# Performance work log

Hardware: AMD Instinct MI355X
Metric: run time of the kernel (lower is better)

Reference implementation:

```python
import jax, jax.numpy as jnp
import numpy as np
from itertools import combinations

WAY = 5
TSS = 3  # temporal_set_size


def setup_inputs() -> dict:
    key = jax.random.key(0)
    k1, k2, k3 = jax.random.split(key, 3)
    n_support, n_queries, seq_len, D = 25, 400, 8, 2048
    d_out = D // 2
    support_set = jax.random.normal(k1, (n_support, seq_len, D), dtype=jnp.float32)
    queries = jax.random.normal(k2, (n_queries, seq_len, D), dtype=jnp.float32)
    support_labels = jnp.arange(n_support, dtype=jnp.int64) % WAY  # shot=5 per class
    W = jax.random.normal(k3, (d_out, TSS * D), dtype=jnp.float32) * 0.02
    b = jnp.zeros((d_out,), dtype=jnp.float32)
    return {"support_set": support_set, "support_labels": support_labels,
            "queries": queries, "W": W, "b": b}


def reference(support_set, support_labels, queries, W, b):
    # Dropout is identity at inference; omitted for determinism.
    n_s, seq_len, D = support_set.shape
    n_q = queries.shape[0]
    tup = jnp.asarray(list(combinations(range(seq_len), TSS)))  # [Tn, 3]
    Tn = tup.shape[0]
    # gather frame tuples and flatten: [N, Tn, 3*D]
    s = support_set[:, tup, :].reshape(n_s, Tn, TSS * D)
    q = queries[:, tup, :].reshape(n_q, Tn, TSS * D)
    # Linear + ReLU embedding
    qe = jax.nn.relu(q.reshape(n_q * Tn, TSS * D) @ W.T + b)          # [Q*Tn, d2]
    se = jax.nn.relu(s.reshape(n_s * Tn, TSS * D) @ W.T + b)
    se = se.reshape(n_s, Tn, -1)
    # group support by class (labels are static ints; shot per class is equal)
    order = jnp.argsort(support_labels, stable=True)                  # sorted by label
    cls_se = se[order.reshape(WAY, -1)].reshape(WAY, -1, se.shape[-1])  # [way, shot*Tn, d2]
    # pairwise Euclidean distances per class: ||q||^2 + ||s||^2 - 2 q.s
    q2 = jnp.sum(qe * qe, axis=-1)                                    # [Q*Tn]
    s2 = jnp.sum(cls_se * cls_se, axis=-1)                            # [way, shot*Tn]
    dots = jnp.einsum('qd,csd->cqs', qe, cls_se)                      # [way, Q*Tn, shot*Tn]
    dist = jnp.sqrt(jnp.maximum(q2[None, :, None] + s2[:, None, :] - 2.0 * dots, 0.0))
    min_dist = dist.min(axis=2).reshape(WAY, n_q, Tn)                 # min over class supports
    logits = -min_dist.mean(axis=2).T                                 # [n_q, way]
    return logits
```

## Files before the change

### kernel.cpp

```cpp
#include <hip/hip_runtime.h>
#include <math.h>

#define NSUP 25
#define NQ   400
#define SL   8
#define DIM  2048
#define DOUT 1024
#define WAY  5
#define TN   56
#define SHOT 5
#define QT   (NQ*TN)
#define STC  (SHOT*TN)
#define NFS  (NSUP*SL)
#define NFQ  (NQ*SL)
#define MF   (NFS+NFQ)
#define MFP  3456
#define PN   (3*DOUT)
#define NSE  1400
#define NSEP 1408

typedef __attribute__((ext_vector_type(8))) short short8;
typedef __attribute__((ext_vector_type(8))) int   int8v;
typedef __attribute__((ext_vector_type(4))) float f32x4;

#define GLOAD_LDS(g, l) __builtin_amdgcn_global_load_lds( \
    (const __attribute__((address_space(1))) unsigned*)(g), \
    (__attribute__((address_space(3))) unsigned*)(l), 16, 0, 0)

__device__ __forceinline__ unsigned short f2bf(float x) {
  unsigned u = __float_as_uint(x);
  u += 0x7fff + ((u >> 16) & 1);
  return (unsigned short)(u >> 16);
}
__device__ __forceinline__ float bf2f(unsigned short h) {
  return __uint_as_float(((unsigned)h) << 16);
}
__device__ __forceinline__ unsigned pk4_fp8(float a, float b, float c, float d) {
  unsigned p = __builtin_amdgcn_cvt_pk_fp8_f32(a, b, 0, false);
  p = __builtin_amdgcn_cvt_pk_fp8_f32(c, d, p, true);
  return p;
}
__device__ __forceinline__ float f8deq(unsigned b) {
  unsigned e = (b >> 3) & 15, m = b & 7;
  return e ? ldexpf((float)(8 + m), (int)e - 10) : ldexpf((float)m, -9);
}

__device__ __constant__ unsigned short TUP[TN] = {
  0x210,0x310,0x410,0x510,0x610,0x710,
  0x320,0x420,0x520,0x620,0x720,
  0x430,0x530,0x630,0x730,
  0x540,0x640,0x740,
  0x650,0x750,
  0x760,
  0x321,0x421,0x521,0x621,0x721,
  0x431,0x531,0x631,0x731,
  0x541,0x641,0x741,
  0x651,0x751,
  0x761,
  0x432,0x532,0x632,0x732,
  0x542,0x642,0x742,
  0x652,0x752,
  0x762,
  0x543,0x643,0x743,
  0x653,0x753,
  0x763,
  0x654,0x754,
  0x764,
  0x765
};

__global__ __launch_bounds__(256) void prep(
    const float* __restrict__ sup, const float* __restrict__ qry,
    const float* __restrict__ W,
    unsigned char* __restrict__ A8, unsigned char* __restrict__ W8,
    unsigned char* __restrict__ se8, float* __restrict__ s2,
    unsigned* __restrict__ pmin)
{
  int idx = blockIdx.x * 256 + threadIdx.x;
  {
    int e = idx * 4;
    int row = e >> 11, c = e & 2047;
    float4 v = make_float4(0.f, 0.f, 0.f, 0.f);
    if (row < NFS)      v = *(const float4*)(sup + (size_t)row * DIM + c);
    else if (row < MF)  v = *(const float4*)(qry + (size_t)(row - NFS) * DIM + c);
    *(unsigned*)(A8 + e) = pk4_fp8(v.x, v.y, v.z, v.w);
  }
  if (idx < PN*DIM/4) {
    int e = idx * 4;
    int n = e >> 11, c = e & 2047;
    const float4 v = *(const float4*)(W + (size_t)(n & 1023) * (3*DIM) + (n >> 10) * DIM + c);
    *(unsigned*)(W8 + e) = pk4_fp8(v.x*64.f, v.y*64.f, v.z*64.f, v.w*64.f);
  }
  if (idx < WAY * QT) pmin[idx] = 0x7F800000u;
  if (idx < (NSEP - NSE) * DOUT) se8[(size_t)NSE * DOUT + idx] = 0;
  if (idx < NSEP - NSE) s2[NSE + idx] = 0.f;
}

__device__ __forceinline__ void mfma_kloop_f8(
    const unsigned char* pa, const unsigned char* pb, int sa, int sb,
    unsigned char* As, unsigned char* Bs,
    int w, int l, int nk, int wm, int wn, int lane15, int quad, f32x4 acc[4][4])
{
  const int r0 = w*32 + (l >> 3), cb = (l & 7) * 16;
  pa += (size_t)r0 * sa + cb;
  pb += (size_t)r0 * sb + cb;
  unsigned char* lA = As + (w*32) * 128;
  unsigned char* lB = Bs + (w*32) * 128;
  for (int kk = 0; kk < nk; ++kk) {
    __syncthreads();
#pragma unroll
    for (int q = 0; q < 4; ++q) {
      GLOAD_LDS(pa + (size_t)q*8*sa, lA + q*1024);
      GLOAD_LDS(pb + (size_t)q*8*sb, lB + q*1024);
    }
    pa += 128; pb += 128;
    __syncthreads();
    int8v af[4], bfr[4];
#pragma unroll
    for (int i = 0; i < 4; ++i) {
      af[i]  = *(const int8v*)(As + (wm + i*16 + lane15)*128 + quad*32);
      bfr[i] = *(const int8v*)(Bs + (wn + i*16 + lane15)*128 + quad*32);
    }
#pragma unroll
    for (int i = 0; i < 4; ++i)
#pragma unroll
      for (int j = 0; j < 4; ++j)
        acc[i][j] = __builtin_amdgcn_mfma_scale_f32_16x16x128_f8f6f4(
            af[i], bfr[j], acc[i][j], 0, 0, 0, 0x7f7f7f7f, 0, 0x7f7f7f7f);
  }
}

__global__ __launch_bounds__(256) void gemm_embed_f8(
    const unsigned char* __restrict__ A8, const unsigned char* __restrict__ W8,
    unsigned short* __restrict__ P)
{
  __shared__ unsigned char As[128*128];
  __shared__ unsigned char Bs[128*128];
  const int bm = blockIdx.x * 128, bn = blockIdx.y * 128;
  const int tid = threadIdx.x, w = tid >> 6, l = tid & 63;
  const int lane15 = l & 15, quad = l >> 4;
  const int wm = (w & 1) * 64, wn = (w >> 1) * 64;

  f32x4 acc[4][4] = {};
  mfma_kloop_f8(A8 + (size_t)bm * DIM, W8 + (size_t)bn * DIM, DIM, DIM,
                As, Bs, w, l, DIM/128, wm, wn, lane15, quad, acc);

#pragma unroll
  for (int i = 0; i < 4; ++i) {
#pragma unroll
    for (int r = 0; r < 4; ++r) {
      int row = bm + wm + i*16 + quad*4 + r;
      if (row < MF) {
#pragma unroll
        for (int j = 0; j < 4; ++j) {
          int col = bn + wn + j*16 + lane15;
          P[(size_t)row * PN + col] = f2bf(acc[i][j][r] * 0.015625f);
        }
      }
    }
  }
}

__global__ __launch_bounds__(256) void assemble_seq(
    const unsigned short* __restrict__ P, const float* __restrict__ bias,
    unsigned char* __restrict__ qe8, float* __restrict__ q2,
    unsigned char* __restrict__ se8, float* __restrict__ s2)
{
  __shared__ unsigned short sP[SL * PN];
  const int b2 = blockIdx.x, b = b2 >> 1, half = b2 & 1;
  const int tid = threadIdx.x, w = tid >> 6, l = tid & 63;

  const size_t base = (size_t)b * SL * PN;
#pragma unroll
  for (int qi = 0; qi < 12; ++qi) {
    int off = (qi * 256 + tid) * 8;
    *(short8*)&sP[off] = *(const short8*)(P + base + off);
  }
  __syncthreads();

  float4 bbv[4];
#pragma unroll
  for (int c = 0; c < 4; ++c)
    bbv[c] = *(const float4*)&bias[l*4 + c*256];

  const bool is_sup = b < NSUP;
  unsigned char* E = is_sup ? se8 : qe8;
  float* nrm = is_sup ? s2 : q2;
  int row_base;
  if (is_sup) { int cc = b % WAY, kk = b / WAY; row_base = cc * STC + kk * TN; }
  else        { row_base = (b - NSUP) * TN; }

  const int t_end = half * 28 + 28;
  for (int t = half * 28 + w; t < t_end; t += 4) {
    unsigned int tp = TUP[t];
    int f0 = tp & 15, f1 = (tp >> 4) & 15, f2 = (tp >> 8) & 15;
    int row = row_base + t;
    float ssq = 0.f;
#pragma unroll
    for (int c = 0; c < 4; ++c) {
      int o = l*4 + c*256;
      ushort4 a = *(const ushort4*)&sP[f0*PN + o];
      ushort4 bq = *(const ushort4*)&sP[f1*PN + DOUT + o];
      ushort4 d = *(const ushort4*)&sP[f2*PN + 2*DOUT + o];
      float z0 = fmaxf(bf2f(a.x) + bf2f(bq.x) + bf2f(d.x) + bbv[c].x, 0.f);
      float z1 = fmaxf(bf2f(a.y) + bf2f(bq.y) + bf2f(d.y) + bbv[c].y, 0.f);
      float z2 = fmaxf(bf2f(a.z) + bf2f(bq.z) + bf2f(d.z) + bbv[c].z, 0.f);
      float z3 = fmaxf(bf2f(a.w) + bf2f(bq.w) + bf2f(d.w) + bbv[c].w, 0.f);
      unsigned pk = pk4_fp8(z0, z1, z2, z3);
      *(unsigned*)&E[(size_t)row * DOUT + o] = pk;
      float x0 = f8deq(pk & 255),         x1 = f8deq((pk >> 8) & 255);
      float x2 = f8deq((pk >> 16) & 255), x3 = f8deq(pk >> 24);
      ssq += x0*x0 + x1*x1 + x2*x2 + x3*x3;
    }
#pragma unroll
    for (int off = 1; off < 64; off <<= 1) ssq += __shfl_xor(ssq, off, 64);
    if (l == 0) nrm[row] = ssq;
  }
}

__global__ __launch_bounds__(256) void gemm_dist_f8(
    const unsigned char* __restrict__ qe8, const unsigned char* __restrict__ se8,
    const float* __restrict__ q2, const float* __restrict__ s2,
    unsigned* __restrict__ pmin)
{
  __shared__ unsigned char As[128*128];
  __shared__ unsigned char Bs[128*128];
  const int bm = blockIdx.x * 128;
  const int bn = blockIdx.y * 128;
  const int tid = threadIdx.x, w = tid >> 6, l = tid & 63;
  const int lane15 = l & 15, quad = l >> 4;
  const int wm = (w & 1) * 64, wn = (w >> 1) * 64;

  f32x4 acc[4][4] = {};
  mfma_kloop_f8(se8 + (size_t)bm * DOUT, qe8 + (size_t)bn * DOUT, DOUT, DOUT,
                As, Bs, w, l, DOUT/128, wm, wn, lane15, quad, acc);

  float s2v[4][4]; int clsv[4][4];
#pragma unroll
  for (int i = 0; i < 4; ++i)
#pragma unroll
    for (int r = 0; r < 4; ++r) {
      int sec = bm + wm + i*16 + quad*4 + r;
      s2v[i][r] = s2[sec];
      clsv[i][r] = sec / STC;
    }
#pragma unroll
  for (int i = 0; i < 4; ++i)
#pragma unroll
    for (int j = 0; j < 4; ++j)
#pragma unroll
      for (int r = 0; r < 4; ++r)
        acc[i][j][r] = fmaf(-2.f, acc[i][j][r], s2v[i][r]);

  float q2v[4];
#pragma unroll
  for (int j = 0; j < 4; ++j)
    q2v[j] = q2[bn + wn + j*16 + lane15];

  const int c_lo = (bm + wm) / STC;
  const int c_hi = min((bm + wm + 63) / STC, WAY - 1);
  for (int c = c_lo; c <= c_hi; ++c) {
#pragma unroll
    for (int j = 0; j < 4; ++j) {
      float mv = INFINITY;
#pragma unroll
      for (int i = 0; i < 4; ++i)
#pragma unroll
        for (int r = 0; r < 4; ++r)
          mv = fminf(mv, (clsv[i][r] == c) ? acc[i][j][r] : INFINITY);
      mv = fminf(mv, __shfl_xor(mv, 16, 64));
      mv = fminf(mv, __shfl_xor(mv, 32, 64));
      if (quad == 0) {
        float val = fmaxf(q2v[j] + mv, 0.f);
        atomicMin(&pmin[(size_t)c * QT + bn + wn + j*16 + lane15],
                  __float_as_uint(val));
      }
    }
  }
}

__global__ void finalize(const unsigned* __restrict__ pmin, float* __restrict__ out)
{
  int idx = blockIdx.x * blockDim.x + threadIdx.x;
  if (idx >= NQ * WAY) return;
  int i = idx / WAY, c = idx % WAY;
  float sum = 0.f;
  for (int t = 0; t < TN; ++t) {
    float v = __uint_as_float(pmin[(size_t)c * QT + i * TN + t]);
    sum += sqrtf(v);
  }
  out[i * WAY + c] = -sum * (1.f / (float)TN);
}

extern "C" void kernel_launch(void* const* d_in, const int* in_sizes, int n_in,
                              void* d_out, int out_size, void* d_ws, size_t ws_size,
                              hipStream_t stream) {
  const float* support = (const float*)d_in[0];
  const float* queries  = (const float*)d_in[2];
  const float* W        = (const float*)d_in[3];
  const float* bias     = (const float*)d_in[4];
  float* out = (float*)d_out;

  char* ws = (char*)d_ws;
  unsigned char* A8 = (unsigned char*)ws;           ws += (size_t)MFP * DIM;
  unsigned char* W8 = (unsigned char*)ws;           ws += (size_t)PN * DIM;
  unsigned short* P = (unsigned short*)ws;          ws += (size_t)MF * PN * 2;
  unsigned char* qe8 = (unsigned char*)ws;          ws += (size_t)QT * DOUT;
  unsigned char* se8 = (unsigned char*)ws;          ws += (size_t)NSEP * DOUT;
  float*         q2  = (float*)ws;                  ws += (size_t)QT * 4;
  float*         s2  = (float*)ws;                  ws += (size_t)NSEP * 4;
  unsigned*      pm  = (unsigned*)ws;

  prep<<<MFP*DIM/4/256, 256, 0, stream>>>(support, queries, W, A8, W8, se8, s2, pm);
  gemm_embed_f8<<<dim3(MFP/128, PN/128), 256, 0, stream>>>(A8, W8, P);
  assemble_seq<<<2*(NSUP + NQ), 256, 0, stream>>>(P, bias, qe8, q2, se8, s2);
  gemm_dist_f8<<<dim3(NSEP/128, QT/128), 256, 0, stream>>>(qe8, se8, q2, s2, pm);
  finalize<<<(NQ*WAY + 255)/256, 256, 0, stream>>>(pm, out);
}
```

Baseline: 220.5 us.

## Use 256x128 FP8 GEMM tiles with swizzled LDS layout and B-fragment reuse

Both FP8 MFMA GEMMs (embedding and distance) now use 256-row A tiles with 8x4 accumulators per wave, which halves the number of blocks and raises arithmetic intensity per LDS load. The LDS layout gets an XOR column swizzle to reduce bank conflicts on fragment reads. B fragments are now loaded one at a time and reused across eight MFMAs. Padding grows and rows are clamped so the larger tiles stay in bounds. The cost is more registers per thread (launch_bounds 256,2), more LDS per block, and fewer blocks, which may under-fill the GPU for the distance GEMM's 6-wide grid.

```diff
diff --git a/kernel.cpp b/kernel.cpp
--- a/kernel.cpp
+++ b/kernel.cpp
@@ -14,7 +14,7 @@
 #define NFS  (NSUP*SL)
 #define NFQ  (NQ*SL)
 #define MF   (NFS+NFQ)
-#define MFP  3456
+#define MFP  3584
 #define PN   (3*DOUT)
 #define NSE  1400
 #define NSEP 1408
@@ -97,56 +97,65 @@
 }
 
 __device__ __forceinline__ void mfma_kloop_f8(
-    const unsigned char* pa, const unsigned char* pb, int sa, int sb,
+    const unsigned char* __restrict__ gA, const unsigned char* __restrict__ gB,
+    int sa, int sb, int rowA0, int rowB0, int clampA,
     unsigned char* As, unsigned char* Bs,
-    int w, int l, int nk, int wm, int wn, int lane15, int quad, f32x4 acc[4][4])
-{
-  const int r0 = w*32 + (l >> 3), cb = (l & 7) * 16;
-  pa += (size_t)r0 * sa + cb;
-  pb += (size_t)r0 * sb + cb;
-  unsigned char* lA = As + (w*32) * 128;
+    int w, int l, int nk, f32x4 acc[8][4])
+{
+  const int lrow = l >> 3;
+  const int cswz = ((((l >> 1) & 3) ^ (lrow & 3)) * 2 + (l & 1)) * 16;
+  unsigned offA[8], offB[4];
+#pragma unroll
+  for (int q = 0; q < 8; ++q)
+    offA[q] = (unsigned)min(rowA0 + w*64 + q*8 + lrow, clampA) * sa + cswz;
+#pragma unroll
+  for (int q = 0; q < 4; ++q)
+    offB[q] = (unsigned)(rowB0 + w*32 + q*8 + lrow) * sb + cswz;
+  unsigned char* lA = As + (w*64) * 128;
   unsigned char* lB = Bs + (w*32) * 128;
-  for (int kk = 0; kk < nk; ++kk) {
+  const int lane15 = l & 15, quad = l >> 4;
+  const int wm = (w & 1) * 128, wn = (w >> 1) * 64;
+  const int slot = (quad ^ (lane15 & 3)) * 32;
+
+  int koff = 0;
+  for (int kk = 0; kk < nk; ++kk, koff += 128) {
     __syncthreads();
 #pragma unroll
-    for (int q = 0; q < 4; ++q) {
-      GLOAD_LDS(pa + (size_t)q*8*sa, lA + q*1024);
-      GLOAD_LDS(pb + (size_t)q*8*sb, lB + q*1024);
-    }
-    pa += 128; pb += 128;
+    for (int q = 0; q < 8; ++q) GLOAD_LDS(gA + offA[q] + koff, lA + q*1024);
+#pragma unroll
+    for (int q = 0; q < 4; ++q) GLOAD_LDS(gB + offB[q] + koff, lB + q*1024);
     __syncthreads();
-    int8v af[4], bfr[4];
-#pragma unroll
-    for (int i = 0; i < 4; ++i) {
-      af[i]  = *(const int8v*)(As + (wm + i*16 + lane15)*128 + quad*32);
-      bfr[i] = *(const int8v*)(Bs + (wn + i*16 + lane15)*128 + quad*32);
-    }
-#pragma unroll
-    for (int i = 0; i < 4; ++i)
-#pragma unroll
-      for (int j = 0; j < 4; ++j)
+    int8v af[8];
+#pragma unroll
+    for (int i = 0; i < 8; ++i)
+      af[i] = *(const int8v*)(As + (wm + i*16 + lane15)*128 + slot);
+#pragma unroll
+    for (int j = 0; j < 4; ++j) {
+      int8v bf = *(const int8v*)(Bs + (wn + j*16 + lane15)*128 + slot);
+#pragma unroll
+      for (int i = 0; i < 8; ++i)
         acc[i][j] = __builtin_amdgcn_mfma_scale_f32_16x16x128_f8f6f4(
-            af[i], bfr[j], acc[i][j], 0, 0, 0, 0x7f7f7f7f, 0, 0x7f7f7f7f);
-  }
-}
-
-__global__ __launch_bounds__(256) void gemm_embed_f8(
+            af[i], bf, acc[i][j], 0, 0, 0, 0x7f7f7f7f, 0, 0x7f7f7f7f);
+    }
+  }
+}
+
+__global__ __launch_bounds__(256, 2) void gemm_embed_f8(
     const unsigned char* __restrict__ A8, const unsigned char* __restrict__ W8,
     unsigned short* __restrict__ P)
 {
-  __shared__ unsigned char As[128*128];
+  __shared__ unsigned char As[256*128];
   __shared__ unsigned char Bs[128*128];
-  const int bm = blockIdx.x * 128, bn = blockIdx.y * 128;
+  const int bm = blockIdx.x * 256, bn = blockIdx.y * 128;
   const int tid = threadIdx.x, w = tid >> 6, l = tid & 63;
   const int lane15 = l & 15, quad = l >> 4;
-  const int wm = (w & 1) * 64, wn = (w >> 1) * 64;
-
-  f32x4 acc[4][4] = {};
-  mfma_kloop_f8(A8 + (size_t)bm * DIM, W8 + (size_t)bn * DIM, DIM, DIM,
-                As, Bs, w, l, DIM/128, wm, wn, lane15, quad, acc);
-
-#pragma unroll
-  for (int i = 0; i < 4; ++i) {
+  const int wm = (w & 1) * 128, wn = (w >> 1) * 64;
+
+  f32x4 acc[8][4] = {};
+  mfma_kloop_f8(A8, W8, DIM, DIM, bm, bn, MFP-1, As, Bs, w, l, DIM/128, acc);
+
+#pragma unroll
+  for (int i = 0; i < 8; ++i) {
 #pragma unroll
     for (int r = 0; r < 4; ++r) {
       int row = bm + wm + i*16 + quad*4 + r;
@@ -218,34 +227,33 @@
   }
 }
 
-__global__ __launch_bounds__(256) void gemm_dist_f8(
+__global__ __launch_bounds__(256, 2) void gemm_dist_f8(
     const unsigned char* __restrict__ qe8, const unsigned char* __restrict__ se8,
     const float* __restrict__ q2, const float* __restrict__ s2,
     unsigned* __restrict__ pmin)
 {
-  __shared__ unsigned char As[128*128];
+  __shared__ unsigned char As[256*128];
   __shared__ unsigned char Bs[128*128];
-  const int bm = blockIdx.x * 128;
+  const int bm = blockIdx.x * 256;
   const int bn = blockIdx.y * 128;
   const int tid = threadIdx.x, w = tid >> 6, l = tid & 63;
   const int lane15 = l & 15, quad = l >> 4;
-  const int wm = (w & 1) * 64, wn = (w >> 1) * 64;
-
-  f32x4 acc[4][4] = {};
-  mfma_kloop_f8(se8 + (size_t)bm * DOUT, qe8 + (size_t)bn * DOUT, DOUT, DOUT,
-                As, Bs, w, l, DOUT/128, wm, wn, lane15, quad, acc);
-
-  float s2v[4][4]; int clsv[4][4];
-#pragma unroll
-  for (int i = 0; i < 4; ++i)
+  const int wm = (w & 1) * 128, wn = (w >> 1) * 64;
+
+  f32x4 acc[8][4] = {};
+  mfma_kloop_f8(se8, qe8, DOUT, DOUT, bm, bn, NSEP-1, As, Bs, w, l, DOUT/128, acc);
+
+  float s2v[8][4]; int clsv[8][4];
+#pragma unroll
+  for (int i = 0; i < 8; ++i)
 #pragma unroll
     for (int r = 0; r < 4; ++r) {
       int sec = bm + wm + i*16 + quad*4 + r;
-      s2v[i][r] = s2[sec];
+      s2v[i][r] = s2[min(sec, NSEP-1)];
       clsv[i][r] = sec / STC;
     }
 #pragma unroll
-  for (int i = 0; i < 4; ++i)
+  for (int i = 0; i < 8; ++i)
 #pragma unroll
     for (int j = 0; j < 4; ++j)
 #pragma unroll
@@ -258,13 +266,13 @@
     q2v[j] = q2[bn + wn + j*16 + lane15];
 
   const int c_lo = (bm + wm) / STC;
-  const int c_hi = min((bm + wm + 63) / STC, WAY - 1);
+  const int c_hi = min((bm + wm + 127) / STC, WAY - 1);
   for (int c = c_lo; c <= c_hi; ++c) {
 #pragma unroll
     for (int j = 0; j < 4; ++j) {
       float mv = INFINITY;
 #pragma unroll
-      for (int i = 0; i < 4; ++i)
+      for (int i = 0; i < 8; ++i)
 #pragma unroll
         for (int r = 0; r < 4; ++r)
           mv = fminf(mv, (clsv[i][r] == c) ? acc[i][j][r] : INFINITY);
@@ -312,8 +320,8 @@
   unsigned*      pm  = (unsigned*)ws;
 
   prep<<<MFP*DIM/4/256, 256, 0, stream>>>(support, queries, W, A8, W8, se8, s2, pm);
-  gemm_embed_f8<<<dim3(MFP/128, PN/128), 256, 0, stream>>>(A8, W8, P);
+  gemm_embed_f8<<<dim3(MFP/256, PN/128), 256, 0, stream>>>(A8, W8, P);
   assemble_seq<<<2*(NSUP + NQ), 256, 0, stream>>>(P, bias, qe8, q2, se8, s2);
-  gemm_dist_f8<<<dim3(NSEP/128, QT/128), 256, 0, stream>>>(qe8, se8, q2, s2, pm);
+  gemm_dist_f8<<<dim3(6, QT/128), 256, 0, stream>>>(qe8, se8, q2, s2, pm);
   finalize<<<(NQ*WAY + 255)/256, 256, 0, stream>>>(pm, out);
 }
```

New measurement: 204.7 us. 1.08x faster.

## Double-buffer LDS tiles with XOR swizzle in FP8 MFMA k-loop

Applied to the files above, without the earlier changes.

Rewrites the shared FP8 MFMA k-loop to double-buffer the A/B LDS tiles, so global-to-LDS loads for the next k-step are issued before computing the current one, and to drop one barrier per iteration. It XOR-swizzles the 16-byte chunk placement in LDS to reduce bank conflicts on fragment reads and clamps A rows to the padded buffer bound. This doubles LDS use per block to 64KB and adds launch_bounds occupancy hints, which may limit blocks per CU.

```diff
diff --git a/kernel.cpp b/kernel.cpp
--- a/kernel.cpp
+++ b/kernel.cpp
@@ -97,53 +97,68 @@
 }
 
 __device__ __forceinline__ void mfma_kloop_f8(
-    const unsigned char* pa, const unsigned char* pb, int sa, int sb,
+    const unsigned char* __restrict__ gA, const unsigned char* __restrict__ gB,
+    int sa, int sb, int rowA0, int rowB0, int clampA,
     unsigned char* As, unsigned char* Bs,
-    int w, int l, int nk, int wm, int wn, int lane15, int quad, f32x4 acc[4][4])
-{
-  const int r0 = w*32 + (l >> 3), cb = (l & 7) * 16;
-  pa += (size_t)r0 * sa + cb;
-  pb += (size_t)r0 * sb + cb;
-  unsigned char* lA = As + (w*32) * 128;
-  unsigned char* lB = Bs + (w*32) * 128;
-  for (int kk = 0; kk < nk; ++kk) {
+    int w, int l, int nk, f32x4 acc[4][4])
+{
+  const int lrow = l >> 3;
+  const int cswz = ((((l >> 1) & 3) ^ (lrow & 3)) * 2 + (l & 1)) * 16;
+  unsigned offA[4], offB[4];
+#pragma unroll
+  for (int q = 0; q < 4; ++q) {
+    offA[q] = (unsigned)min(rowA0 + w*32 + q*8 + lrow, clampA) * sa + cswz;
+    offB[q] = (unsigned)(rowB0 + w*32 + q*8 + lrow) * sb + cswz;
+  }
+  const int lw = (w*32) * 128;
+  const int lane15 = l & 15, quad = l >> 4;
+  const int wm = (w & 1) * 64, wn = (w >> 1) * 64;
+  const int slot = (quad ^ (lane15 & 3)) * 32;
+
+#pragma unroll
+  for (int q = 0; q < 4; ++q) {
+    GLOAD_LDS(gA + offA[q], As + lw + q*1024);
+    GLOAD_LDS(gB + offB[q], Bs + lw + q*1024);
+  }
+  int koff = 128;
+  for (int kk = 0; kk < nk; ++kk, koff += 128) {
     __syncthreads();
-#pragma unroll
-    for (int q = 0; q < 4; ++q) {
-      GLOAD_LDS(pa + (size_t)q*8*sa, lA + q*1024);
-      GLOAD_LDS(pb + (size_t)q*8*sb, lB + q*1024);
-    }
-    pa += 128; pb += 128;
-    __syncthreads();
-    int8v af[4], bfr[4];
+    const int cur = (kk & 1) * 16384, nxt = 16384 - cur;
+    if (kk + 1 < nk) {
+#pragma unroll
+      for (int q = 0; q < 4; ++q) {
+        GLOAD_LDS(gA + offA[q] + koff, As + nxt + lw + q*1024);
+        GLOAD_LDS(gB + offB[q] + koff, Bs + nxt + lw + q*1024);
+      }
+    }
+    int8v af[4], bf[4];
 #pragma unroll
     for (int i = 0; i < 4; ++i) {
-      af[i]  = *(const int8v*)(As + (wm + i*16 + lane15)*128 + quad*32);
-      bfr[i] = *(const int8v*)(Bs + (wn + i*16 + lane15)*128 + quad*32);
+      af[i] = *(const int8v*)(As + cur + (wm + i*16 + lane15)*128 + slot);
+      bf[i] = *(const int8v*)(Bs + cur + (wn + i*16 + lane15)*128 + slot);
     }
 #pragma unroll
     for (int i = 0; i < 4; ++i)
 #pragma unroll
       for (int j = 0; j < 4; ++j)
         acc[i][j] = __builtin_amdgcn_mfma_scale_f32_16x16x128_f8f6f4(
-            af[i], bfr[j], acc[i][j], 0, 0, 0, 0x7f7f7f7f, 0, 0x7f7f7f7f);
-  }
-}
-
-__global__ __launch_bounds__(256) void gemm_embed_f8(
+            af[i], bf[j], acc[i][j], 0, 0, 0, 0x7f7f7f7f, 0, 0x7f7f7f7f);
+  }
+}
+
+__global__ __launch_bounds__(256, 2) void gemm_embed_f8(
     const unsigned char* __restrict__ A8, const unsigned char* __restrict__ W8,
     unsigned short* __restrict__ P)
 {
-  __shared__ unsigned char As[128*128];
-  __shared__ unsigned char Bs[128*128];
+  __shared__ unsigned char As[2*128*128];
+  __shared__ unsigned char Bs[2*128*128];
   const int bm = blockIdx.x * 128, bn = blockIdx.y * 128;
   const int tid = threadIdx.x, w = tid >> 6, l = tid & 63;
   const int lane15 = l & 15, quad = l >> 4;
   const int wm = (w & 1) * 64, wn = (w >> 1) * 64;
 
   f32x4 acc[4][4] = {};
-  mfma_kloop_f8(A8 + (size_t)bm * DIM, W8 + (size_t)bn * DIM, DIM, DIM,
-                As, Bs, w, l, DIM/128, wm, wn, lane15, quad, acc);
+  mfma_kloop_f8(A8, W8, DIM, DIM, bm, bn, MFP-1, As, Bs, w, l, DIM/128, acc);
 
 #pragma unroll
   for (int i = 0; i < 4; ++i) {
@@ -218,13 +233,13 @@
   }
 }
 
-__global__ __launch_bounds__(256) void gemm_dist_f8(
+__global__ __launch_bounds__(256, 2) void gemm_dist_f8(
     const unsigned char* __restrict__ qe8, const unsigned char* __restrict__ se8,
     const float* __restrict__ q2, const float* __restrict__ s2,
     unsigned* __restrict__ pmin)
 {
-  __shared__ unsigned char As[128*128];
-  __shared__ unsigned char Bs[128*128];
+  __shared__ unsigned char As[2*128*128];
+  __shared__ unsigned char Bs[2*128*128];
   const int bm = blockIdx.x * 128;
   const int bn = blockIdx.y * 128;
   const int tid = threadIdx.x, w = tid >> 6, l = tid & 63;
@@ -232,8 +247,7 @@
   const int wm = (w & 1) * 64, wn = (w >> 1) * 64;
 
   f32x4 acc[4][4] = {};
-  mfma_kloop_f8(se8 + (size_t)bm * DOUT, qe8 + (size_t)bn * DOUT, DOUT, DOUT,
-                As, Bs, w, l, DOUT/128, wm, wn, lane15, quad, acc);
+  mfma_kloop_f8(se8, qe8, DOUT, DOUT, bm, bn, NSEP-1, As, Bs, w, l, DOUT/128, acc);
 
   float s2v[4][4]; int clsv[4][4];
 #pragma unroll
```

Result: slower. 540.9 us (+145.3%).
